# Kernel optimization log

Measured on AMD Instinct MI355X. Metric: run time of the kernel, lower is better.

Reference implementation:

```python
import jax, jax.numpy as jnp
import numpy as np


def setup_inputs() -> dict:
    key = jax.random.key(0)
    k1, k2 = jax.random.split(key)
    b, t_x, d = 16, 1024, 256
    max_dur = 8
    x = jax.random.normal(k1, (b, t_x, d), dtype=jnp.float32)
    repeat_count = jax.random.randint(k2, (b, t_x), 0, max_dur, dtype=jnp.int64)
    out_len = t_x * (max_dur - 1)  # static upper bound on max(cumsum(durations))
    return {"x": x, "repeat_count": repeat_count, "out_len": out_len}


def reference(x, repeat_count, out_len):
    # x: (b, t_x, d); repeat_count: (b, t_x) int; out_len: static int (t_y)
    cum = jnp.cumsum(repeat_count.astype(jnp.int64), axis=1)          # (b, t_x)
    # content mask: M[b, i, j] = 1 if j < cum[b, i]
    cols = jnp.arange(out_len)                                        # (t_y,)
    M = (cols[None, None, :] < cum[:, :, None]).astype(x.dtype)       # (b, t_x, t_y)
    # row-wise diff along t_x turns prefix masks into per-phoneme one-hot spans
    M = jnp.concatenate([M[:, :1, :], M[:, 1:, :] - M[:, :-1, :]], axis=1)
    # bmm(M^T, x): expand phonemes into frames
    out = jnp.einsum('bxt,bxd->btd', M, x)                            # (b, t_y, d)
    lengths = jnp.max(cum, axis=1)                                    # (b,)
    return out, lengths
```

## Files before the change

kernel.cpp:

```cpp
#include <hip/hip_runtime.h>

#define B       16
#define TX      1024
#define D       256
#define OUT_LEN 7168
#define TILE    16

__global__ __launch_bounds__(256) void lr_scan_kernel(
        const int* __restrict__ rc,
        int* __restrict__ cum,
        float* __restrict__ len_out)
{
    __shared__ int part[256];
    const int b = blockIdx.x;
    const int t = threadIdx.x;

    const int4* rc4 = (const int4*)(rc + b * TX);
    int4 v = rc4[t];
    const int s0 = v.x;
    const int s1 = s0 + v.y;
    const int s2 = s1 + v.z;
    const int s3 = s2 + v.w;

    part[t] = s3;
    __syncthreads();

    #pragma unroll
    for (int off = 1; off < 256; off <<= 1) {
        int tmp = (t >= off) ? part[t - off] : 0;
        __syncthreads();
        part[t] += tmp;
        __syncthreads();
    }

    const int excl = part[t] - s3;
    int4 c;
    c.x = excl + s0;
    c.y = excl + s1;
    c.z = excl + s2;
    c.w = excl + s3;
    ((int4*)(cum + b * TX))[t] = c;

    if (t == 255) {
        len_out[b] = (float)part[255];
    }
}

__global__ __launch_bounds__(256) void lr_expand_kernel(
        const float* __restrict__ x,
        const int* __restrict__ cum,
        float* __restrict__ out)
{
    __shared__ int scum[TX];

    const int blocks_per_batch = OUT_LEN / TILE;
    const int b    = blockIdx.x / blocks_per_batch;
    const int row0 = (blockIdx.x % blocks_per_batch) * TILE;
    const int t    = threadIdx.x;

    ((int4*)scum)[t] = ((const int4*)(cum + b * TX))[t];
    __syncthreads();

    const int total = scum[TX - 1];
    const int lane4 = t & 63;
    const int sub   = t >> 6;

    const float4* x4   = (const float4*)(x + (size_t)b * TX * D);
    float4*       out4 = (float4*)(out + (size_t)b * OUT_LEN * D);

    #pragma unroll
    for (int r = sub; r < TILE; r += 4) {
        const int j = row0 + r;
        float4 val = make_float4(0.f, 0.f, 0.f, 0.f);
        if (j < total) {
            int i = 0;
            #pragma unroll
            for (int step = TX / 2; step > 0; step >>= 1) {
                if (scum[i + step - 1] <= j) i += step;
            }
            val = x4[(size_t)i * (D / 4) + lane4];
        }
        out4[(size_t)j * (D / 4) + lane4] = val;
    }
}

extern "C" void kernel_launch(void* const* d_in, const int* in_sizes, int n_in,
                              void* d_out, int out_size, void* d_ws, size_t ws_size,
                              hipStream_t stream) {
    const float* x  = (const float*)d_in[0];
    const int*   rc = (const int*)d_in[1];
    float* out = (float*)d_out;
    float* len_out = out + (size_t)B * OUT_LEN * D;
    int* cum = (int*)d_ws;

    lr_scan_kernel<<<B, 256, 0, stream>>>(rc, cum, len_out);

    const int grid = B * (OUT_LEN / TILE);
    lr_expand_kernel<<<grid, 256, 0, stream>>>(x, cum, out);
}
```

Measured before the change: 139.1 us.

## Precompute per-frame source index map in scan kernel instead of binary search

The scan kernel now uses a wavefront-shuffle scan and scatters the source phoneme index for every output frame into a 16-bit lookup table, with 0xFFFF marking padding frames. The expand kernel reads that index directly. This removes the per-block 4 KB cumsum staging into LDS and the 10-step binary search per row. Loads and stores of x and out are also made nontemporal to avoid polluting the caches. The trade-off is a serial per-thread scatter loop and a full-table fill in the small scan kernel.

Result: slower. 144.4 us (+3.8%).

```diff
diff --git a/kernel.cpp b/kernel.cpp
--- a/kernel.cpp
+++ b/kernel.cpp
@@ -6,81 +6,86 @@
 #define OUT_LEN 7168
 #define TILE    16
 
-__global__ __launch_bounds__(256) void lr_scan_kernel(
+typedef float v4f __attribute__((ext_vector_type(4)));
+
+__global__ __launch_bounds__(256) void lr_scan_scatter_kernel(
         const int* __restrict__ rc,
-        int* __restrict__ cum,
+        unsigned short* __restrict__ src,
         float* __restrict__ len_out)
 {
-    __shared__ int part[256];
+    __shared__ int wtot[4];
     const int b = blockIdx.x;
     const int t = threadIdx.x;
 
-    const int4* rc4 = (const int4*)(rc + b * TX);
-    int4 v = rc4[t];
+    const int4 v = ((const int4*)(rc + b * TX))[t];
     const int s0 = v.x;
     const int s1 = s0 + v.y;
     const int s2 = s1 + v.z;
     const int s3 = s2 + v.w;
 
-    part[t] = s3;
+    uint2* srow8 = (uint2*)(src + (size_t)b * OUT_LEN);
+    const uint2 ff = make_uint2(0xFFFFFFFFu, 0xFFFFFFFFu);
+    #pragma unroll
+    for (int k = 0; k < OUT_LEN / (4 * 256); ++k)
+        srow8[t + 256 * k] = ff;
+
+    int wscan = s3;
+    #pragma unroll
+    for (int off = 1; off < 64; off <<= 1) {
+        int n = __shfl_up(wscan, off, 64);
+        if ((t & 63) >= off) wscan += n;
+    }
+    if ((t & 63) == 63) wtot[t >> 6] = wscan;
     __syncthreads();
 
+    int wexcl = 0;
     #pragma unroll
-    for (int off = 1; off < 256; off <<= 1) {
-        int tmp = (t >= off) ? part[t - off] : 0;
-        __syncthreads();
-        part[t] += tmp;
-        __syncthreads();
-    }
+    for (int w = 0; w < 3; ++w)
+        if (w < (t >> 6)) wexcl += wtot[w];
+    const int incl = wexcl + wscan;
+    const int excl = incl - s3;
 
-    const int excl = part[t] - s3;
-    int4 c;
-    c.x = excl + s0;
-    c.y = excl + s1;
-    c.z = excl + s2;
-    c.w = excl + s3;
-    ((int4*)(cum + b * TX))[t] = c;
+    if (t == 255) len_out[b] = (float)incl;
 
-    if (t == 255) {
-        len_out[b] = (float)part[255];
-    }
+    unsigned short* s = src + (size_t)b * OUT_LEN;
+    const int i0 = 4 * t;
+    const int ofs[4] = {excl, excl + s0, excl + s1, excl + s2};
+    const int cnt[4] = {v.x, v.y, v.z, v.w};
+    #pragma unroll
+    for (int e = 0; e < 4; ++e)
+        for (int k = 0; k < cnt[e]; ++k)
+            s[ofs[e] + k] = (unsigned short)(i0 + e);
 }
 
 __global__ __launch_bounds__(256) void lr_expand_kernel(
         const float* __restrict__ x,
-        const int* __restrict__ cum,
+        const unsigned short* __restrict__ src,
         float* __restrict__ out)
 {
-    __shared__ int scum[TX];
-
     const int blocks_per_batch = OUT_LEN / TILE;
     const int b    = blockIdx.x / blocks_per_batch;
     const int row0 = (blockIdx.x % blocks_per_batch) * TILE;
     const int t    = threadIdx.x;
-
-    ((int4*)scum)[t] = ((const int4*)(cum + b * TX))[t];
-    __syncthreads();
-
-    const int total = scum[TX - 1];
     const int lane4 = t & 63;
     const int sub   = t >> 6;
 
-    const float4* x4   = (const float4*)(x + (size_t)b * TX * D);
-    float4*       out4 = (float4*)(out + (size_t)b * OUT_LEN * D);
+    const v4f* x4 = (const v4f*)(x + (size_t)b * TX * D);
+    v4f*     out4 = (v4f*)(out + (size_t)b * OUT_LEN * D);
+    const unsigned short* srow = src + (size_t)b * OUT_LEN + row0;
+
+    int idx[4];
+    #pragma unroll
+    for (int e = 0; e < 4; ++e)
+        idx[e] = srow[sub + 4 * e];
 
     #pragma unroll
-    for (int r = sub; r < TILE; r += 4) {
-        const int j = row0 + r;
-        float4 val = make_float4(0.f, 0.f, 0.f, 0.f);
-        if (j < total) {
-            int i = 0;
-            #pragma unroll
-            for (int step = TX / 2; step > 0; step >>= 1) {
-                if (scum[i + step - 1] <= j) i += step;
-            }
-            val = x4[(size_t)i * (D / 4) + lane4];
-        }
-        out4[(size_t)j * (D / 4) + lane4] = val;
+    for (int e = 0; e < 4; ++e) {
+        const int j = row0 + sub + 4 * e;
+        const int i = idx[e];
+        v4f val = (v4f)(0.f);
+        if (i != 0xFFFF)
+            val = __builtin_nontemporal_load(&x4[(size_t)i * (D / 4) + lane4]);
+        __builtin_nontemporal_store(val, &out4[(size_t)j * (D / 4) + lane4]);
     }
 }
 
@@ -91,10 +96,10 @@
     const int*   rc = (const int*)d_in[1];
     float* out = (float*)d_out;
     float* len_out = out + (size_t)B * OUT_LEN * D;
-    int* cum = (int*)d_ws;
+    unsigned short* src = (unsigned short*)d_ws;
 
-    lr_scan_kernel<<<B, 256, 0, stream>>>(rc, cum, len_out);
+    lr_scan_scatter_kernel<<<B, 256, 0, stream>>>(rc, src, len_out);
 
     const int grid = B * (OUT_LEN / TILE);
-    lr_expand_kernel<<<grid, 256, 0, stream>>>(x, cum, out);
+    lr_expand_kernel<<<grid, 256, 0, stream>>>(x, src, out);
 }
```
